# Performance work log

Hardware: AMD Instinct MI355X
Metric: run time of the kernel (lower is better)

The kernel has to match this reference:

```python
import jax, jax.numpy as jnp
import numpy as np

D_MODEL = 1024
N_HEADS = 16
HEAD_DIM = D_MODEL // N_HEADS
D_FF = 4096
EPS = 1e-5


def setup_inputs() -> dict:
    key = jax.random.key(0)
    ks = jax.random.split(key, 12)
    s = 0.02
    return {
        "x": jax.random.normal(ks[0], (2, 2048, D_MODEL), jnp.float32),
        "wq": jax.random.normal(ks[1], (D_MODEL, D_MODEL), jnp.float32) * s,
        "bq": jnp.zeros((D_MODEL,), jnp.float32),
        "wk": jax.random.normal(ks[2], (D_MODEL, D_MODEL), jnp.float32) * s,
        "bk": jnp.zeros((D_MODEL,), jnp.float32),
        "wv": jax.random.normal(ks[3], (D_MODEL, D_MODEL), jnp.float32) * s,
        "bv": jnp.zeros((D_MODEL,), jnp.float32),
        "wo": jax.random.normal(ks[4], (D_MODEL, D_MODEL), jnp.float32) * s,
        "bo": jnp.zeros((D_MODEL,), jnp.float32),
        "w1": jax.random.normal(ks[5], (D_MODEL, D_FF), jnp.float32) * s,
        "b1": jnp.zeros((D_FF,), jnp.float32),
        "w2": jax.random.normal(ks[6], (D_FF, D_MODEL), jnp.float32) * s,
        "b2": jnp.zeros((D_MODEL,), jnp.float32),
        "g1": jnp.ones((D_MODEL,), jnp.float32),
        "be1": jnp.zeros((D_MODEL,), jnp.float32),
        "g2": jnp.ones((D_MODEL,), jnp.float32),
        "be2": jnp.zeros((D_MODEL,), jnp.float32),
    }


def _layer_norm(x, g, b):
    mu = jnp.mean(x, axis=-1, keepdims=True)
    var = jnp.var(x, axis=-1, keepdims=True)
    return (x - mu) * jax.lax.rsqrt(var + EPS) * g + b


def reference(x, wq, bq, wk, bk, wv, bv, wo, bo, w1, b1, w2, b2, g1, be1, g2, be2):
    B, S, D = x.shape
    nx = _layer_norm(x, g1, be1)
    # projections -> [B, H, S, d]
    def split_heads(t):
        return t.reshape(B, S, N_HEADS, HEAD_DIM).transpose(0, 2, 1, 3)
    q = split_heads(nx @ wq + bq)
    k = split_heads(nx @ wk + bk)
    v = split_heads(nx @ wv + bv)
    scores = jnp.einsum("bhqd,bhkd->bhqk", q, k) / jnp.sqrt(jnp.float32(HEAD_DIM))
    attn = jax.nn.softmax(scores, axis=-1)
    out = jnp.einsum("bhqk,bhkd->bhqd", attn, v)
    out = out.transpose(0, 2, 1, 3).reshape(B, S, D)
    x = x + (out @ wo + bo)
    nx = _layer_norm(x, g2, be2)
    ff = jax.nn.relu(nx @ w1 + b1) @ w2 + b2
    return x + ff
```

## Files before the change

kernel.cpp:

```cpp
#include <hip/hip_runtime.h>


typedef __attribute__((ext_vector_type(8))) unsigned short u16x8;
typedef __attribute__((ext_vector_type(4))) unsigned short u16x4;
typedef __attribute__((ext_vector_type(8))) __bf16 bf16x8;
typedef __attribute__((ext_vector_type(4))) float f32x4;
typedef __attribute__((ext_vector_type(4))) unsigned int u32x4;

#define C_SCALE 0.1803368801111f

static __device__ __forceinline__ unsigned short f2b(float f) {
    return __builtin_bit_cast(unsigned short, (__bf16)f);
}
static __device__ __forceinline__ float b2f(unsigned short h) {
    unsigned u = ((unsigned)h) << 16;
    float f;
    __builtin_memcpy(&f, &u, 4);
    return f;
}

static __device__ __forceinline__ void async_cp16(
    const unsigned short* g, unsigned short* l)
{
    __builtin_amdgcn_global_load_lds(
        (const __attribute__((address_space(1))) unsigned int*)g,
        (__attribute__((address_space(3))) unsigned int*)l,
        16, 0, 0);
}

__global__ __launch_bounds__(256) void prep_all_k(
    const float* __restrict__ wq, const float* __restrict__ wk,
    const float* __restrict__ wv, const float* __restrict__ wo,
    const float* __restrict__ w1, const float* __restrict__ w2,
    unsigned short* __restrict__ wqkvT, unsigned short* __restrict__ woT,
    unsigned short* __restrict__ w1T, unsigned short* __restrict__ w2T,
    const float* __restrict__ bq, const float* __restrict__ bk,
    const float* __restrict__ bv, float* __restrict__ bqkv,
    const float* __restrict__ x, const float* __restrict__ g1,
    const float* __restrict__ be1, unsigned short* __restrict__ lnout)
{
    __shared__ unsigned short tile[32][33];
    __shared__ float sb[4], ssb[4];
    const int ti = blockIdx.x;

    if (ti < 12288) {
        const float* in;
        unsigned short* out;
        int R, C, bi, bj;
        float sc = 1.0f;
        if (ti < 4096) {
            R = 1024; C = 1024;
            bi = (ti & 1023) >> 5; bj = ti & 31;
            int z = ti >> 10;
            in = (z == 0) ? wq : (z == 1) ? wk : (z == 2) ? wv : wo;
            out = (z < 3) ? wqkvT + (size_t)z * 1024 * 1024 : woT;
            if (z == 1) sc = C_SCALE;
        } else if (ti < 8192) {
            R = 1024; C = 4096;
            int l = ti - 4096;
            bi = l >> 7; bj = l & 127;
            in = w1; out = w1T;
        } else {
            R = 4096; C = 1024;
            int l = ti - 8192;
            bi = l >> 5; bj = l & 31;
            in = w2; out = w2T;
        }
        const int tx = threadIdx.x & 31, ty = threadIdx.x >> 5;
#pragma unroll
        for (int rr = 0; rr < 4; ++rr) {
            int r = ty + rr * 8;
            tile[r][tx] = f2b(in[(size_t)(bi * 32 + r) * C + bj * 32 + tx] * sc);
        }
        __syncthreads();
#pragma unroll
        for (int rr = 0; rr < 4; ++rr) {
            int r = ty + rr * 8;
            out[(size_t)(bj * 32 + r) * R + bi * 32 + tx] = tile[tx][r];
        }
        return;
    }
    if (ti < 12300) {
        int t = (ti - 12288) * 256 + threadIdx.x;
        float v = (t < 1024) ? bq[t]
                : ((t < 2048) ? bk[t - 1024] * C_SCALE : bv[t - 2048]);
        bqkv[t] = v;
        return;
    }
    const int row = ti - 12300;
    const int t = threadIdx.x;
    const float* xr = x + (size_t)row * 1024;
    float4 v4 = *reinterpret_cast<const float4*>(&xr[t * 4]);
    float f[4] = {v4.x, v4.y, v4.z, v4.w};
    float s = f[0] + f[1] + f[2] + f[3];
    float ss = f[0] * f[0] + f[1] * f[1] + f[2] * f[2] + f[3] * f[3];
#pragma unroll
    for (int d = 1; d < 64; d <<= 1) {
        s += __shfl_xor(s, d);
        ss += __shfl_xor(ss, d);
    }
    const int wave = t >> 6;
    if ((t & 63) == 0) { sb[wave] = s; ssb[wave] = ss; }
    __syncthreads();
    s = sb[0] + sb[1] + sb[2] + sb[3];
    ss = ssb[0] + ssb[1] + ssb[2] + ssb[3];
    const float mu = s * (1.0f / 1024.0f);
    const float var = ss * (1.0f / 1024.0f) - mu * mu;
    const float rs = rsqrtf(var + 1e-5f);
    u16x4 r4;
#pragma unroll
    for (int j = 0; j < 4; ++j)
        r4[j] = f2b((f[j] - mu) * rs * g1[t * 4 + j] + be1[t * 4 + j]);
    *reinterpret_cast<u16x4*>(&lnout[(size_t)row * 1024 + t * 4]) = r4;
}

__global__ __launch_bounds__(256) void reduce_ln_kernel(
    const unsigned short* __restrict__ pa, const unsigned short* __restrict__ pb,
    const float* __restrict__ bias, const float* __restrict__ x,
    const float* __restrict__ g, const float* __restrict__ be,
    float* __restrict__ x2, unsigned short* __restrict__ o)
{
    const int row = blockIdx.x;
    const int t = threadIdx.x;
    const size_t base = (size_t)row * 1024 + t * 4;
    float4 x4 = *reinterpret_cast<const float4*>(&x[base]);
    float4 bb = *reinterpret_cast<const float4*>(&bias[t * 4]);
    float f[4] = {x4.x + bb.x, x4.y + bb.y, x4.z + bb.z, x4.w + bb.w};
#pragma unroll
    for (int z = 0; z < 2; ++z) {
        u16x4 va = *reinterpret_cast<const u16x4*>(&pa[(size_t)z * 4096 * 1024 + base]);
        u16x4 vb = *reinterpret_cast<const u16x4*>(&pb[(size_t)z * 4096 * 1024 + base]);
#pragma unroll
        for (int j = 0; j < 4; ++j) f[j] += b2f(va[j]) + b2f(vb[j]);
    }
    *reinterpret_cast<float4*>(&x2[base]) = {f[0], f[1], f[2], f[3]};
    float s = f[0] + f[1] + f[2] + f[3];
    float ss = f[0] * f[0] + f[1] * f[1] + f[2] * f[2] + f[3] * f[3];
#pragma unroll
    for (int d = 1; d < 64; d <<= 1) {
        s += __shfl_xor(s, d);
        ss += __shfl_xor(ss, d);
    }
    __shared__ float sb[4], ssb[4];
    const int wave = t >> 6;
    if ((t & 63) == 0) { sb[wave] = s; ssb[wave] = ss; }
    __syncthreads();
    s = sb[0] + sb[1] + sb[2] + sb[3];
    ss = ssb[0] + ssb[1] + ssb[2] + ssb[3];
    const float mu = s * (1.0f / 1024.0f);
    const float var = ss * (1.0f / 1024.0f) - mu * mu;
    const float rs = rsqrtf(var + 1e-5f);
    u16x4 r4;
#pragma unroll
    for (int j = 0; j < 4; ++j)
        r4[j] = f2b((f[j] - mu) * rs * g[t * 4 + j] + be[t * 4 + j]);
    *reinterpret_cast<u16x4*>(&o[base]) = r4;
}

__global__ __launch_bounds__(256) void reduce_out4_k(
    const unsigned short* __restrict__ pa, const unsigned short* __restrict__ pb,
    const float* __restrict__ bias, const float* __restrict__ x2,
    float* __restrict__ out)
{
    const size_t i4 = ((size_t)blockIdx.x * 256 + threadIdx.x) * 4;
    float4 x4 = *reinterpret_cast<const float4*>(&x2[i4]);
    float4 bb = *reinterpret_cast<const float4*>(&bias[i4 & 1023]);
    float a0 = x4.x + bb.x, a1 = x4.y + bb.y, a2 = x4.z + bb.z, a3 = x4.w + bb.w;
#pragma unroll
    for (int z = 0; z < 2; ++z) {
        u16x4 va = *reinterpret_cast<const u16x4*>(&pa[(size_t)z * 4096 * 1024 + i4]);
        u16x4 vb = *reinterpret_cast<const u16x4*>(&pb[(size_t)z * 4096 * 1024 + i4]);
        a0 += b2f(va[0]) + b2f(vb[0]);
        a1 += b2f(va[1]) + b2f(vb[1]);
        a2 += b2f(va[2]) + b2f(vb[2]);
        a3 += b2f(va[3]) + b2f(vb[3]);
    }
    *reinterpret_cast<float4*>(&out[i4]) = {a0, a1, a2, a3};
}

template<int MODE, int RELU>
__global__ __launch_bounds__(512, 1) void gemm256(
    const unsigned short* __restrict__ A, int lda,
    const unsigned short* __restrict__ Bt, int ldb,
    const float* __restrict__ bias,
    void* __restrict__ Cv, void* __restrict__ Cv2, int N, int Kloop)
{
    __shared__ unsigned short lds[3 * 16384];
    const int t = threadIdx.x;
    const int wave = t >> 6, lane = t & 63;
    const int quad = lane >> 4, l16 = lane & 15;
    const int wm = wave >> 2, wn = wave & 3;
    const int nwg = gridDim.x * gridDim.y;
    const int id = blockIdx.y * gridDim.x + blockIdx.x;
    const int sw = (id & 7) * (nwg >> 3) + (id >> 3);
    const int m0 = (sw / gridDim.x) * 256;
    const int n0 = (sw % gridDim.x) * 256;
    const int k0 = blockIdx.z * Kloop;
    const int NT = Kloop >> 5;

    const int sc_row = t >> 2;
    const int sc_cb  = (t & 3) ^ ((t >> 3) & 3);
    const unsigned short* Asrc = &A[(size_t)(m0 + sc_row) * lda + k0 + sc_cb * 8];
    const unsigned short* Bsrc = &Bt[(size_t)(n0 + sc_row) * ldb + k0 + sc_cb * 8];
    const size_t Astep = (size_t)128 * lda;
    const size_t Bstep = (size_t)128 * ldb;
    unsigned short* dstA = &lds[t * 8];
    unsigned short* dstB = &lds[8192 + t * 8];

    const int cb = quad ^ ((l16 >> 1) & 3);
    const int aoff = (wm * 128 + l16) * 32 + cb * 8;
    const int boff = 8192 + (wn * 64 + l16) * 32 + cb * 8;

    f32x4 acc[8][4];
#pragma unroll
    for (int mi = 0; mi < 8; ++mi)
#pragma unroll
        for (int ni = 0; ni < 4; ++ni) acc[mi][ni] = {0.f, 0.f, 0.f, 0.f};

    async_cp16(Asrc, dstA);
    async_cp16(Asrc + Astep, dstA + 4096);
    async_cp16(Bsrc, dstB);
    async_cp16(Bsrc + Bstep, dstB + 4096);
    if (NT > 1) {
        async_cp16(Asrc + 32, dstA + 16384);
        async_cp16(Asrc + Astep + 32, dstA + 16384 + 4096);
        async_cp16(Bsrc + 32, dstB + 16384);
        async_cp16(Bsrc + Bstep + 32, dstB + 16384 + 4096);
        asm volatile("s_waitcnt vmcnt(4)\n\ts_barrier" ::: "memory");
    } else {
        asm volatile("s_waitcnt vmcnt(0)\n\ts_barrier" ::: "memory");
    }

    for (int tt = 0; tt < NT; ++tt) {
        const int b = tt - (tt / 3) * 3;
        const unsigned short* Lb = &lds[b * 16384];
        const int pf = tt + 2;
        const int bp = (pf < NT) ? (pf - (pf / 3) * 3) * 16384 : 0;
        bf16x8 af[8], bfr[4];
        if (pf < NT) {
            async_cp16(Asrc + (size_t)pf * 32, &lds[bp] + t * 8);
            async_cp16(Asrc + Astep + (size_t)pf * 32, &lds[bp] + t * 8 + 4096);
        }
#pragma unroll
        for (int mi = 0; mi < 8; ++mi)
            af[mi] = __builtin_bit_cast(bf16x8,
                *reinterpret_cast<const u16x8*>(&Lb[aoff + mi * 512]));
        bfr[0] = __builtin_bit_cast(bf16x8,
            *reinterpret_cast<const u16x8*>(&Lb[boff]));
        bfr[1] = __builtin_bit_cast(bf16x8,
            *reinterpret_cast<const u16x8*>(&Lb[boff + 512]));
        __builtin_amdgcn_s_setprio(1);
#pragma unroll
        for (int mi = 0; mi < 8; ++mi) {
            acc[mi][0] = __builtin_amdgcn_mfma_f32_16x16x32_bf16(
                af[mi], bfr[0], acc[mi][0], 0, 0, 0);
            acc[mi][1] = __builtin_amdgcn_mfma_f32_16x16x32_bf16(
                af[mi], bfr[1], acc[mi][1], 0, 0, 0);
        }
        __builtin_amdgcn_s_setprio(0);
        if (pf < NT) {
            async_cp16(Bsrc + (size_t)pf * 32, &lds[bp + 8192] + t * 8);
            async_cp16(Bsrc + Bstep + (size_t)pf * 32, &lds[bp + 8192] + t * 8 + 4096);
        }
        bfr[2] = __builtin_bit_cast(bf16x8,
            *reinterpret_cast<const u16x8*>(&Lb[boff + 1024]));
        bfr[3] = __builtin_bit_cast(bf16x8,
            *reinterpret_cast<const u16x8*>(&Lb[boff + 1536]));
        __builtin_amdgcn_s_setprio(1);
#pragma unroll
        for (int mi = 0; mi < 8; ++mi) {
            acc[mi][2] = __builtin_amdgcn_mfma_f32_16x16x32_bf16(
                af[mi], bfr[2], acc[mi][2], 0, 0, 0);
            acc[mi][3] = __builtin_amdgcn_mfma_f32_16x16x32_bf16(
                af[mi], bfr[3], acc[mi][3], 0, 0, 0);
        }
        __builtin_amdgcn_s_setprio(0);
        if (tt + 1 < NT) {
            if (pf < NT)
                asm volatile("s_waitcnt vmcnt(4)\n\ts_barrier" ::: "memory");
            else
                asm volatile("s_waitcnt vmcnt(0)\n\ts_barrier" ::: "memory");
        }
    }

#pragma unroll
    for (int mi = 0; mi < 8; ++mi) {
        const int gr0 = m0 + wm * 128 + mi * 16 + quad * 4;
#pragma unroll
        for (int ni = 0; ni < 4; ++ni) {
            const int gc = n0 + wn * 64 + ni * 16 + l16;
            if (MODE == 2) {
                const float bv = bias[gc];
                if (gc < 2048) {
#pragma unroll
                    for (int r = 0; r < 4; ++r)
                        ((unsigned short*)Cv)[(size_t)(gr0 + r) * 2048 + gc] =
                            f2b(acc[mi][ni][r] + bv);
                } else {
                    u16x4 pk;
#pragma unroll
                    for (int r = 0; r < 4; ++r) pk[r] = f2b(acc[mi][ni][r] + bv);
                    const int bb = gr0 >> 11, s0 = gr0 & 2047;
                    *reinterpret_cast<u16x4*>(
                        &((unsigned short*)Cv2)[((size_t)bb * 1024 + (gc - 2048)) * 2048 + s0]) = pk;
                }
            } else if (MODE == 5) {
                unsigned short* base = (blockIdx.z < 2)
                    ? (unsigned short*)Cv  + (size_t)blockIdx.z * 4096 * N
                    : (unsigned short*)Cv2 + (size_t)(blockIdx.z - 2) * 4096 * N;
#pragma unroll
                for (int r = 0; r < 4; ++r)
                    base[(size_t)(gr0 + r) * N + gc] = f2b(acc[mi][ni][r]);
            } else {
                const float bv = bias[gc];
#pragma unroll
                for (int r = 0; r < 4; ++r) {
                    float v = acc[mi][ni][r] + bv;
                    if (RELU) v = fmaxf(v, 0.f);
                    ((unsigned short*)Cv)[(size_t)(gr0 + r) * N + gc] = f2b(v);
                }
            }
        }
    }
}

__global__ __launch_bounds__(256, 2) void attn_kernel(
    const unsigned short* __restrict__ qkb, const unsigned short* __restrict__ vbT,
    unsigned short* __restrict__ ao)
{
    __shared__ unsigned short lds[3 * 8192];
    const int t = threadIdx.x;
    const int lane = t & 63;
    const int quad = lane >> 4, l16 = lane & 15;
    const int wave = t >> 6;
    const int bh = blockIdx.y;
    const int b = bh >> 4, h = bh & 15;
    const int q0 = blockIdx.x * 128 + wave * 32;
    const size_t qk_base = (size_t)b * 2048 * 2048;
    const size_t vt_base = (size_t)b * 1024 * 2048 + (size_t)h * 64 * 2048;

    bf16x8 qf[2][2];
#pragma unroll
    for (int m = 0; m < 2; ++m)
#pragma unroll
        for (int kk = 0; kk < 2; ++kk)
            qf[m][kk] = __builtin_bit_cast(bf16x8, *reinterpret_cast<const u16x8*>(
                &qkb[qk_base + (size_t)(q0 + m * 16 + l16) * 2048 + h * 64 + kk * 32 + quad * 8]));

    u16x8 ones_u;
#pragma unroll
    for (int j = 0; j < 8; ++j) ones_u[j] = 0x3F80;
    const bf16x8 onesf = __builtin_bit_cast(bf16x8, ones_u);

    f32x4 o_acc[2][4], l_frag[2];
#pragma unroll
    for (int m = 0; m < 2; ++m) {
        l_frag[m] = {0.f, 0.f, 0.f, 0.f};
#pragma unroll
        for (int nf = 0; nf < 4; ++nf) o_acc[m][nf] = {0.f, 0.f, 0.f, 0.f};
    }

    const int c0 = t, c1 = t + 256;
    const int r0 = c0 >> 3, r1 = c1 >> 3;
    const int scb0 = (c0 & 7) ^ (r0 & 7), scb1 = (c1 & 7) ^ (r1 & 7);
    const unsigned short* kS0 = &qkb[qk_base + (size_t)r0 * 2048 + 1024 + h * 64 + scb0 * 8];
    const unsigned short* kS1 = &qkb[qk_base + (size_t)r1 * 2048 + 1024 + h * 64 + scb1 * 8];
    const unsigned short* vS0 = &vbT[vt_base + (size_t)r0 * 2048 + scb0 * 8];
    const unsigned short* vS1 = &vbT[vt_base + (size_t)r1 * 2048 + scb1 * 8];

    const int off0 = l16 * 64 + ((quad ^ (l16 & 7)) * 8);

#define STAGE(tile, buf)                                                      \
    {                                                                         \
        const size_t ko = (size_t)(tile) * 64 * 2048;                         \
        const int vo = (tile) * 64;                                           \
        async_cp16(kS0 + ko, &lds[(buf) * 8192 + c0 * 8]);                    \
        async_cp16(kS1 + ko, &lds[(buf) * 8192 + c1 * 8]);                    \
        async_cp16(vS0 + vo, &lds[(buf) * 8192 + 4096 + c0 * 8]);             \
        async_cp16(vS1 + vo, &lds[(buf) * 8192 + 4096 + c1 * 8]);             \
    }

    STAGE(0, 0);
    STAGE(1, 1);
    asm volatile("s_waitcnt vmcnt(4)\n\ts_barrier" ::: "memory");

    for (int tt = 0; tt < 32; ++tt) {
        const int buf = tt - (tt / 3) * 3;
        const int pf = tt + 2;
        if (pf < 32) {
            const int bp = pf - (pf / 3) * 3;
            STAGE(pf, bp);
        }
        const unsigned short* LK = &lds[buf * 8192];
        const unsigned short* LV = LK + 4096;

        unsigned d0[2][4], d1[2][4];
#pragma unroll
        for (int kf = 0; kf < 4; ++kf) {
            bf16x8 kfr0 = __builtin_bit_cast(bf16x8,
                *reinterpret_cast<const u16x8*>(&LK[off0 + kf * 1024]));
            bf16x8 kfr1 = __builtin_bit_cast(bf16x8,
                *reinterpret_cast<const u16x8*>(&LK[(off0 ^ 32) + kf * 1024]));
#pragma unroll
            for (int m = 0; m < 2; ++m) {
                f32x4 s = {0.f, 0.f, 0.f, 0.f};
                s = __builtin_amdgcn_mfma_f32_16x16x32_bf16(kfr0, qf[m][0], s, 0, 0, 0);
                s = __builtin_amdgcn_mfma_f32_16x16x32_bf16(kfr1, qf[m][1], s, 0, 0, 0);
                d0[m][kf] = (unsigned)f2b(exp2f(s[0])) |
                            ((unsigned)f2b(exp2f(s[1])) << 16);
                d1[m][kf] = (unsigned)f2b(exp2f(s[2])) |
                            ((unsigned)f2b(exp2f(s[3])) << 16);
            }
        }
#pragma unroll
        for (int kh = 0; kh < 2; ++kh) {
            bf16x8 pfr[2];
#pragma unroll
            for (int m = 0; m < 2; ++m) {
                unsigned x0 = d0[m][kh * 2], y0 = d0[m][kh * 2 + 1];
                unsigned x1 = d1[m][kh * 2], y1 = d1[m][kh * 2 + 1];
                asm("v_permlane32_swap_b32 %0, %1\n\t"
                    "v_permlane16_swap_b32 %0, %1"
                    : "+v"(x0), "+v"(y0));
                asm("v_permlane32_swap_b32 %0, %1\n\t"
                    "v_permlane16_swap_b32 %0, %1"
                    : "+v"(x1), "+v"(y1));
                u32x4 pw = {x0, x1, y0, y1};
                pfr[m] = __builtin_bit_cast(bf16x8, pw);
                l_frag[m] = __builtin_amdgcn_mfma_f32_16x16x32_bf16(
                    pfr[m], onesf, l_frag[m], 0, 0, 0);
            }
            __builtin_amdgcn_s_setprio(1);
#pragma unroll
            for (int nf = 0; nf < 4; ++nf) {
                bf16x8 vfr = __builtin_bit_cast(bf16x8,
                    *reinterpret_cast<const u16x8*>(&LV[(off0 ^ (kh * 32)) + nf * 1024]));
#pragma unroll
                for (int m = 0; m < 2; ++m)
                    o_acc[m][nf] = __builtin_amdgcn_mfma_f32_16x16x32_bf16(
                        pfr[m], vfr, o_acc[m][nf], 0, 0, 0);
            }
            __builtin_amdgcn_s_setprio(0);
        }
        if (tt + 1 < 32) {
            if (pf < 32)
                asm volatile("s_waitcnt vmcnt(4)\n\ts_barrier" ::: "memory");
            else
                asm volatile("s_waitcnt vmcnt(0)\n\ts_barrier" ::: "memory");
        }
    }
#undef STAGE

#pragma unroll
    for (int m = 0; m < 2; ++m) {
#pragma unroll
        for (int r = 0; r < 4; ++r) {
            const float inv = 1.0f / l_frag[m][r];
            const int row = q0 + m * 16 + quad * 4 + r;
#pragma unroll
            for (int nf = 0; nf < 4; ++nf)
                ao[(size_t)b * 2048 * 1024 + (size_t)row * 1024 + h * 64 + nf * 16 + l16] =
                    f2b(o_acc[m][nf][r] * inv);
        }
    }
}

extern "C" void kernel_launch(void* const* d_in, const int* in_sizes, int n_in,
                              void* d_out, int out_size, void* d_ws, size_t ws_size,
                              hipStream_t stream)
{
    const float* x   = (const float*)d_in[0];
    const float* wq  = (const float*)d_in[1];
    const float* bq  = (const float*)d_in[2];
    const float* wk  = (const float*)d_in[3];
    const float* bk  = (const float*)d_in[4];
    const float* wv  = (const float*)d_in[5];
    const float* bv  = (const float*)d_in[6];
    const float* wo  = (const float*)d_in[7];
    const float* bo  = (const float*)d_in[8];
    const float* w1  = (const float*)d_in[9];
    const float* b1  = (const float*)d_in[10];
    const float* w2  = (const float*)d_in[11];
    const float* b2  = (const float*)d_in[12];
    const float* g1  = (const float*)d_in[13];
    const float* be1 = (const float*)d_in[14];
    const float* g2  = (const float*)d_in[15];
    const float* be2 = (const float*)d_in[16];
    float* out = (float*)d_out;
    char*  ws  = (char*)d_ws;

    const int M = 4096, D = 1024, DFF = 4096;
    const size_t MB = 1 << 20;

    unsigned short* wqkvT = (unsigned short*)(ws + 0 * MB);
    unsigned short* woT   = (unsigned short*)(ws + 6 * MB);
    unsigned short* w1T   = (unsigned short*)(ws + 8 * MB);
    unsigned short* w2T   = (unsigned short*)(ws + 16 * MB);
    unsigned short* ln    = (unsigned short*)(ws + 24 * MB);
    unsigned short* qkb   = (unsigned short*)(ws + 32 * MB);
    unsigned short* vbT   = (unsigned short*)(ws + 48 * MB);
    unsigned short* ao    = (unsigned short*)(ws + 56 * MB);
    unsigned short* ff1   = (unsigned short*)(ws + 32 * MB);
    float*          x2    = (float*)(ws + 64 * MB);
    float*          bqkv  = (float*)(ws + 80 * MB);
    unsigned short* pHi   = (unsigned short*)(ws + 80 * MB);
    unsigned short* pOlo  = (unsigned short*)(ws + 32 * MB);
    unsigned short* pFlo  = (unsigned short*)(ws + 0 * MB);

    prep_all_k<<<16396, 256, 0, stream>>>(wq, wk, wv, wo, w1, w2,
                                          wqkvT, woT, w1T, w2T,
                                          bq, bk, bv, bqkv,
                                          x, g1, be1, ln);
    gemm256<2, 0><<<dim3(12, 16), 512, 0, stream>>>(
        ln, D, wqkvT, D, bqkv, qkb, vbT, 3072, D);
    attn_kernel<<<dim3(16, 32), 256, 0, stream>>>(qkb, vbT, ao);
    gemm256<5, 0><<<dim3(4, 16, 4), 512, 0, stream>>>(
        ao, D, woT, D, nullptr, pHi, pOlo, 1024, 256);
    reduce_ln_kernel<<<M, 256, 0, stream>>>(pHi, pOlo, bo, x, g2, be2, x2, ln);
    gemm256<0, 1><<<dim3(16, 16), 512, 0, stream>>>(
        ln, D, w1T, D, b1, ff1, nullptr, DFF, D);
    gemm256<5, 0><<<dim3(4, 16, 4), 512, 0, stream>>>(
        ff1, DFF, w2T, DFF, nullptr, pHi, pFlo, 1024, 1024);
    reduce_out4_k<<<4096, 256, 0, stream>>>(pHi, pFlo, b2, x2, out);
}
```

Before: 345.0 us.

## Restructure GEMM main loop into 64-wide K steps with four-phase ping-pong pipeline

The 256x256 bf16 GEMM main loop changes from a 3-stage ring of 32-wide K tiles to a double-buffered pair of 64-wide K steps using four LDS buffers. Each iteration runs four phases of 4x4 MFMA blocks. Each phase issues async global-to-LDS copies for part of a future tile and is separated from its neighbours by explicit s_barrier and lgkmcnt waits. The aim is to interleave loads, LDS reads and MFMA more finely and halve the per-K-step loop overhead. The cost is more LDS (128KB) and many more barriers per iteration, which may stall waves.

```diff
diff --git a/kernel.cpp b/kernel.cpp
--- a/kernel.cpp
+++ b/kernel.cpp
@@ -185,7 +185,7 @@
     const float* __restrict__ bias,
     void* __restrict__ Cv, void* __restrict__ Cv2, int N, int Kloop)
 {
-    __shared__ unsigned short lds[3 * 16384];
+    __shared__ unsigned short lds[4 * 16384];
     const int t = threadIdx.x;
     const int wave = t >> 6, lane = t & 63;
     const int quad = lane >> 4, l16 = lane & 15;
@@ -196,16 +196,29 @@
     const int m0 = (sw / gridDim.x) * 256;
     const int n0 = (sw % gridDim.x) * 256;
     const int k0 = blockIdx.z * Kloop;
-    const int NT = Kloop >> 5;
+    const int NT = Kloop >> 6;
 
     const int sc_row = t >> 2;
     const int sc_cb  = (t & 3) ^ ((t >> 3) & 3);
-    const unsigned short* Asrc = &A[(size_t)(m0 + sc_row) * lda + k0 + sc_cb * 8];
-    const unsigned short* Bsrc = &Bt[(size_t)(n0 + sc_row) * ldb + k0 + sc_cb * 8];
+    const unsigned short* Abase = &A[(size_t)(m0 + sc_row) * lda + k0 + sc_cb * 8];
+    const unsigned short* Bbase = &Bt[(size_t)(n0 + sc_row) * ldb + k0 + sc_cb * 8];
     const size_t Astep = (size_t)128 * lda;
     const size_t Bstep = (size_t)128 * ldb;
-    unsigned short* dstA = &lds[t * 8];
-    unsigned short* dstB = &lds[8192 + t * 8];
+
+#define SG(MAT, kh, Tt)                                                       \
+    {                                                                         \
+        unsigned short* d = &lds[(((Tt) & 1) * 2 + (kh)) * 16384 +            \
+                                 ((MAT) ? 8192 : 0) + t * 8];                 \
+        if (MAT) {                                                            \
+            const unsigned short* s = Bbase + (Tt) * 64 + (kh) * 32;          \
+            async_cp16(s, d);                                                 \
+            async_cp16(s + Bstep, d + 4096);                                  \
+        } else {                                                              \
+            const unsigned short* s = Abase + (Tt) * 64 + (kh) * 32;          \
+            async_cp16(s, d);                                                 \
+            async_cp16(s + Astep, d + 4096);                                  \
+        }                                                                     \
+    }
 
     const int cb = quad ^ ((l16 >> 1) & 3);
     const int aoff = (wm * 128 + l16) * 32 + cb * 8;
@@ -217,71 +230,93 @@
 #pragma unroll
         for (int ni = 0; ni < 4; ++ni) acc[mi][ni] = {0.f, 0.f, 0.f, 0.f};
 
-    async_cp16(Asrc, dstA);
-    async_cp16(Asrc + Astep, dstA + 4096);
-    async_cp16(Bsrc, dstB);
-    async_cp16(Bsrc + Bstep, dstB + 4096);
+    SG(0, 0, 0); SG(1, 0, 0); SG(0, 1, 0); SG(1, 1, 0);
     if (NT > 1) {
-        async_cp16(Asrc + 32, dstA + 16384);
-        async_cp16(Asrc + Astep + 32, dstA + 16384 + 4096);
-        async_cp16(Bsrc + 32, dstB + 16384);
-        async_cp16(Bsrc + Bstep + 32, dstB + 16384 + 4096);
+        SG(0, 0, 1); SG(1, 0, 1);
         asm volatile("s_waitcnt vmcnt(4)\n\ts_barrier" ::: "memory");
     } else {
         asm volatile("s_waitcnt vmcnt(0)\n\ts_barrier" ::: "memory");
     }
 
-    for (int tt = 0; tt < NT; ++tt) {
-        const int b = tt - (tt / 3) * 3;
-        const unsigned short* Lb = &lds[b * 16384];
-        const int pf = tt + 2;
-        const int bp = (pf < NT) ? (pf - (pf / 3) * 3) * 16384 : 0;
-        bf16x8 af[8], bfr[4];
-        if (pf < NT) {
-            async_cp16(Asrc + (size_t)pf * 32, &lds[bp] + t * 8);
-            async_cp16(Asrc + Astep + (size_t)pf * 32, &lds[bp] + t * 8 + 4096);
-        }
-#pragma unroll
-        for (int mi = 0; mi < 8; ++mi)
+    for (int T = 0; T < NT; ++T) {
+        const unsigned short* L0 = &lds[((T & 1) * 2 + 0) * 16384];
+        const unsigned short* L1 = &lds[((T & 1) * 2 + 1) * 16384];
+        bf16x8 af[4], bfr[4];
+#pragma unroll
+        for (int mi = 0; mi < 4; ++mi)
             af[mi] = __builtin_bit_cast(bf16x8,
-                *reinterpret_cast<const u16x8*>(&Lb[aoff + mi * 512]));
-        bfr[0] = __builtin_bit_cast(bf16x8,
-            *reinterpret_cast<const u16x8*>(&Lb[boff]));
-        bfr[1] = __builtin_bit_cast(bf16x8,
-            *reinterpret_cast<const u16x8*>(&Lb[boff + 512]));
+                *reinterpret_cast<const u16x8*>(&L0[aoff + mi * 512]));
+#pragma unroll
+        for (int ni = 0; ni < 4; ++ni)
+            bfr[ni] = __builtin_bit_cast(bf16x8,
+                *reinterpret_cast<const u16x8*>(&L0[boff + ni * 512]));
+        if (T + 1 < NT) SG(0, 1, T + 1);
+        asm volatile("s_barrier\n\ts_waitcnt lgkmcnt(0)" ::: "memory");
         __builtin_amdgcn_s_setprio(1);
 #pragma unroll
-        for (int mi = 0; mi < 8; ++mi) {
-            acc[mi][0] = __builtin_amdgcn_mfma_f32_16x16x32_bf16(
-                af[mi], bfr[0], acc[mi][0], 0, 0, 0);
-            acc[mi][1] = __builtin_amdgcn_mfma_f32_16x16x32_bf16(
-                af[mi], bfr[1], acc[mi][1], 0, 0, 0);
-        }
+        for (int mi = 0; mi < 4; ++mi)
+#pragma unroll
+            for (int ni = 0; ni < 4; ++ni)
+                acc[mi][ni] = __builtin_amdgcn_mfma_f32_16x16x32_bf16(
+                    af[mi], bfr[ni], acc[mi][ni], 0, 0, 0);
         __builtin_amdgcn_s_setprio(0);
-        if (pf < NT) {
-            async_cp16(Bsrc + (size_t)pf * 32, &lds[bp + 8192] + t * 8);
-            async_cp16(Bsrc + Bstep + (size_t)pf * 32, &lds[bp + 8192] + t * 8 + 4096);
-        }
-        bfr[2] = __builtin_bit_cast(bf16x8,
-            *reinterpret_cast<const u16x8*>(&Lb[boff + 1024]));
-        bfr[3] = __builtin_bit_cast(bf16x8,
-            *reinterpret_cast<const u16x8*>(&Lb[boff + 1536]));
+        asm volatile("s_barrier" ::: "memory");
+#pragma unroll
+        for (int mi = 0; mi < 4; ++mi)
+            af[mi] = __builtin_bit_cast(bf16x8,
+                *reinterpret_cast<const u16x8*>(&L0[aoff + (mi + 4) * 512]));
+        if (T + 1 < NT) SG(1, 1, T + 1);
+        asm volatile("s_barrier\n\ts_waitcnt lgkmcnt(0)" ::: "memory");
         __builtin_amdgcn_s_setprio(1);
 #pragma unroll
-        for (int mi = 0; mi < 8; ++mi) {
-            acc[mi][2] = __builtin_amdgcn_mfma_f32_16x16x32_bf16(
-                af[mi], bfr[2], acc[mi][2], 0, 0, 0);
-            acc[mi][3] = __builtin_amdgcn_mfma_f32_16x16x32_bf16(
-                af[mi], bfr[3], acc[mi][3], 0, 0, 0);
-        }
+        for (int mi = 0; mi < 4; ++mi)
+#pragma unroll
+            for (int ni = 0; ni < 4; ++ni)
+                acc[mi + 4][ni] = __builtin_amdgcn_mfma_f32_16x16x32_bf16(
+                    af[mi], bfr[ni], acc[mi + 4][ni], 0, 0, 0);
         __builtin_amdgcn_s_setprio(0);
-        if (tt + 1 < NT) {
-            if (pf < NT)
+        asm volatile("s_barrier" ::: "memory");
+#pragma unroll
+        for (int mi = 0; mi < 4; ++mi)
+            af[mi] = __builtin_bit_cast(bf16x8,
+                *reinterpret_cast<const u16x8*>(&L1[aoff + mi * 512]));
+#pragma unroll
+        for (int ni = 0; ni < 4; ++ni)
+            bfr[ni] = __builtin_bit_cast(bf16x8,
+                *reinterpret_cast<const u16x8*>(&L1[boff + ni * 512]));
+        if (T + 2 < NT) SG(0, 0, T + 2);
+        asm volatile("s_barrier\n\ts_waitcnt lgkmcnt(0)" ::: "memory");
+        __builtin_amdgcn_s_setprio(1);
+#pragma unroll
+        for (int mi = 0; mi < 4; ++mi)
+#pragma unroll
+            for (int ni = 0; ni < 4; ++ni)
+                acc[mi][ni] = __builtin_amdgcn_mfma_f32_16x16x32_bf16(
+                    af[mi], bfr[ni], acc[mi][ni], 0, 0, 0);
+        __builtin_amdgcn_s_setprio(0);
+        asm volatile("s_barrier" ::: "memory");
+#pragma unroll
+        for (int mi = 0; mi < 4; ++mi)
+            af[mi] = __builtin_bit_cast(bf16x8,
+                *reinterpret_cast<const u16x8*>(&L1[aoff + (mi + 4) * 512]));
+        if (T + 2 < NT) SG(1, 0, T + 2);
+        asm volatile("s_barrier\n\ts_waitcnt lgkmcnt(0)" ::: "memory");
+        __builtin_amdgcn_s_setprio(1);
+#pragma unroll
+        for (int mi = 0; mi < 4; ++mi)
+#pragma unroll
+            for (int ni = 0; ni < 4; ++ni)
+                acc[mi + 4][ni] = __builtin_amdgcn_mfma_f32_16x16x32_bf16(
+                    af[mi], bfr[ni], acc[mi + 4][ni], 0, 0, 0);
+        __builtin_amdgcn_s_setprio(0);
+        if (T + 1 < NT) {
+            if (T + 2 < NT)
                 asm volatile("s_waitcnt vmcnt(4)\n\ts_barrier" ::: "memory");
             else
                 asm volatile("s_waitcnt vmcnt(0)\n\ts_barrier" ::: "memory");
         }
     }
+#undef SG
 
 #pragma unroll
     for (int mi = 0; mi < 8; ++mi) {
```

Result: no change. 348.5 us (+1.0%).
